# Kernel optimization log

Hardware: AMD Instinct MI355X
Metric: run time of the kernel (lower is better)

## Reference

```python
import jax, jax.numpy as jnp
import numpy as np

B, S, E, H = 2, 2048, 1024, 16
D = E // H  # head_dim = 64


def setup_inputs() -> dict:
    key = jax.random.key(0)
    ks = jax.random.split(key, 9)
    s = 1.0 / np.sqrt(E)
    return {
        "x": jax.random.normal(ks[0], (B, S, E), dtype=jnp.float32),
        "Wq": jax.random.uniform(ks[1], (E, E), jnp.float32, -s, s),
        "bq": jax.random.uniform(ks[2], (E,), jnp.float32, -s, s),
        "Wk": jax.random.uniform(ks[3], (E, E), jnp.float32, -s, s),
        "bk": jax.random.uniform(ks[4], (E,), jnp.float32, -s, s),
        "Wv": jax.random.uniform(ks[5], (E, E), jnp.float32, -s, s),
        "bv": jax.random.uniform(ks[6], (E,), jnp.float32, -s, s),
        "Wo": jax.random.uniform(ks[7], (E, E), jnp.float32, -s, s),
        "bo": jax.random.uniform(ks[8], (E,), jnp.float32, -s, s),
    }


def reference(x, Wq, bq, Wk, bk, Wv, bv, Wo, bo):
    # QKV projections (torch Linear: x @ W.T + b), split into heads: [B,H,S,D]
    def proj(t, W, b):
        return (t @ W.T + b).reshape(B, S, H, D).transpose(0, 2, 1, 3)

    Q = proj(x, Wq, bq)
    K = proj(x, Wk, bk)
    V = proj(x, Wv, bv)
    # scores [B,H,S,S], scaled by sqrt(head_dim)
    score = jnp.einsum('bnqd,bnkd->bnqk', Q, K) / jnp.sqrt(jnp.float32(D))
    weights = jax.nn.softmax(score, axis=-1)
    out = jnp.einsum('bnql,bnld->bnqd', weights, V)  # [B,H,S,D]
    out = out.transpose(0, 2, 1, 3).reshape(B, S, E)
    return out @ Wo.T + bo
```

## Files before the change

kernel.cpp:

```cpp
#include <hip/hip_runtime.h>


#define B_ 2
#define S_ 2048
#define E_ 1024
#define H_ 16
#define D_ 64
#define M_ (B_ * S_)

typedef __attribute__((ext_vector_type(8))) _Float16 f16x8;
typedef __attribute__((ext_vector_type(4))) _Float16 f16x4;
typedef __attribute__((ext_vector_type(2))) _Float16 f16x2;
typedef __attribute__((ext_vector_type(4))) float f32x4;
typedef __attribute__((ext_vector_type(16))) float f32x16;
typedef __attribute__((ext_vector_type(8))) unsigned short u16x8;
typedef __attribute__((ext_vector_type(4))) unsigned int u32x4;

#define LOG2E  1.44269504f
#define CLOG2  4.32808512f

#define KROW 144
#define KBUF 9216
#define VBASE 18432
#define SMEMSZ 36864

static __device__ __forceinline__ float bf16_to_f32(unsigned short u) {
    return __uint_as_float(((unsigned)u) << 16);
}
static __device__ __forceinline__ unsigned short f32_to_bf16(float f) {
    unsigned u = __float_as_uint(f);
    u += 0x7FFFu + ((u >> 16) & 1u);
    return (unsigned short)(u >> 16);
}
static __device__ __forceinline__ float load1_f32(const void* p, int i, bool isbf) {
    return isbf ? bf16_to_f32(((const unsigned short*)p)[i]) : ((const float*)p)[i];
}
static __device__ __forceinline__ void store1(void* p, size_t i, float v, bool isbf) {
    if (isbf) ((unsigned short*)p)[i] = f32_to_bf16(v);
    else      ((float*)p)[i] = v;
}
static __device__ __forceinline__ void gl2lds16(const void* g, void* l) {
    __builtin_amdgcn_global_load_lds((const __attribute__((address_space(1))) unsigned int*)g,
                                     (__attribute__((address_space(3))) unsigned int*)l, 16, 0, 0);
}
static __device__ __forceinline__ float rexp2(float x) {
    float r;
    asm("v_exp_f32 %0, %1" : "=v"(r) : "v"(x));
    return r;
}
static __device__ __forceinline__ unsigned pk2(float a, float b) {
    return __builtin_bit_cast(unsigned, __builtin_amdgcn_cvt_pkrtz(a, b));
}

__global__ __launch_bounds__(256) void convert_inputs(
    const void* __restrict__ x,  const void* __restrict__ wq,
    const void* __restrict__ wk, const void* __restrict__ wv,
    const void* __restrict__ wo,
    _Float16* __restrict__ x16, _Float16* __restrict__ w16,
    int* __restrict__ flag_out)
{
    __shared__ int sflag;
    const int tid = threadIdx.x;
    if (tid < 64) {
        const unsigned short hh = ((const unsigned short*)x)[2 * tid];
        const int e = (hh >> 7) & 0xFF;
        const bool sane = (e >= 0x60 && e <= 0x9F);
        const unsigned long long m = __ballot(sane);
        if (tid == 0) sflag = (__popcll(m) >= 48) ? 1 : 0;
    }
    __syncthreads();
    const bool isbf = sflag != 0;
    if (blockIdx.x == 0 && tid == 0) *flag_out = sflag;

    const size_t t = ((size_t)blockIdx.x * 256 + tid) * 8;
    const void* src; size_t off; _Float16* dst; float scale = 1.0f;
    if (t < (size_t)M_ * E_) { src = x; off = t; dst = x16 + t; }
    else {
        const size_t u = t - (size_t)M_ * E_;
        const int wsel = (int)(u >> 20);
        off = u & ((1u << 20) - 1);
        src = wsel == 0 ? wq : wsel == 1 ? wk : wsel == 2 ? wv : wo;
        dst = w16 + u;
        if (wsel == 0) scale = 0.125f * LOG2E;
    }
    f16x8 v;
    if (isbf) {
        u16x8 s = *(const u16x8*)((const unsigned short*)src + off);
        #pragma unroll
        for (int j = 0; j < 8; ++j) v[j] = (_Float16)(bf16_to_f32(s[j]) * scale);
    } else {
        const float* f = (const float*)src + off;
        f32x4 lo = *(const f32x4*)f;
        f32x4 hi = *(const f32x4*)(f + 4);
        #pragma unroll
        for (int j = 0; j < 4; ++j) {
            v[j]     = (_Float16)(lo[j] * scale);
            v[4 + j] = (_Float16)(hi[j] * scale);
        }
    }
    *(f16x8*)dst = v;
}

__global__ __launch_bounds__(256) void gemm_qkv(
    const _Float16* __restrict__ x16, const _Float16* __restrict__ w16,
    const void* __restrict__ bq, const void* __restrict__ bk, const void* __restrict__ bv,
    const int* __restrict__ flag,
    _Float16* __restrict__ Qb, _Float16* __restrict__ Kb, _Float16* __restrict__ VTb)
{
    __shared__ __align__(16) _Float16 Xs[128 * 64];
    __shared__ __align__(16) _Float16 Ws[64 * 64];
    const bool isbf = (*flag != 0);
    const int tid = threadIdx.x, wave = tid >> 6, lane = tid & 63;
    const int wm = wave >> 1, wn = wave & 1;
    const int qd = lane >> 4, ln = lane & 15;
    const int m0 = blockIdx.x * 128;
    const int by = blockIdx.y;
    const int wsel = by >> 4;
    const int n0 = (by & 15) * 64;
    const _Float16* W = w16 + ((size_t)wsel << 20);

    const _Float16* gx[4]; char* lx[4];
    #pragma unroll
    for (int it = 0; it < 4; ++it) {
        const int seg = it * 256 + tid;
        const int row = seg >> 3, cg = seg & 7;
        const int scol = ((cg + row) & 7) * 8;
        gx[it] = x16 + (size_t)(m0 + row) * E_ + scol;
        lx[it] = (char*)Xs + (size_t)(it * 256 + wave * 64) * 16;
    }
    const _Float16* gw[2]; char* lw[2];
    #pragma unroll
    for (int it = 0; it < 2; ++it) {
        const int seg = it * 256 + tid;
        const int row = seg >> 3, cg = seg & 7;
        const int scol = ((cg + row) & 7) * 8;
        gw[it] = W + (size_t)(n0 + row) * E_ + scol;
        lw[it] = (char*)Ws + (size_t)(it * 256 + wave * 64) * 16;
    }

    const int sw0 = ((qd - ln) & 7) * 8;
    const int sw1 = ((qd + 4 - ln) & 7) * 8;

    f32x4 acc[8] = {};

    for (int kt = 0; kt < E_; kt += 64) {
        __syncthreads();
        #pragma unroll
        for (int it = 0; it < 4; ++it) gl2lds16(gx[it] + kt, lx[it]);
        #pragma unroll
        for (int it = 0; it < 2; ++it) gl2lds16(gw[it] + kt, lw[it]);
        __syncthreads();
        if (wsel != 2) {
            #pragma unroll
            for (int kk = 0; kk < 2; ++kk) {
                const int sw = kk ? sw1 : sw0;
                f16x8 a[4], bfr[2];
                #pragma unroll
                for (int mt = 0; mt < 4; ++mt)
                    a[mt] = *(const f16x8*)&Xs[((wm * 64 + mt * 16 + ln) << 6) + sw];
                #pragma unroll
                for (int nt = 0; nt < 2; ++nt)
                    bfr[nt] = *(const f16x8*)&Ws[((wn * 32 + nt * 16 + ln) << 6) + sw];
                #pragma unroll
                for (int mt = 0; mt < 4; ++mt)
                    #pragma unroll
                    for (int nt = 0; nt < 2; ++nt)
                        acc[mt * 2 + nt] = __builtin_amdgcn_mfma_f32_16x16x32_f16(a[mt], bfr[nt], acc[mt * 2 + nt], 0, 0, 0);
            }
        } else {
            #pragma unroll
            for (int kk = 0; kk < 2; ++kk) {
                const int sw = kk ? sw1 : sw0;
                f16x8 a[2], bfr[4];
                #pragma unroll
                for (int mt = 0; mt < 2; ++mt)
                    a[mt] = *(const f16x8*)&Ws[((wm * 32 + mt * 16 + ln) << 6) + sw];
                #pragma unroll
                for (int nt = 0; nt < 4; ++nt)
                    bfr[nt] = *(const f16x8*)&Xs[((wn * 64 + nt * 16 + ln) << 6) + sw];
                #pragma unroll
                for (int mt = 0; mt < 2; ++mt)
                    #pragma unroll
                    for (int nt = 0; nt < 4; ++nt)
                        acc[mt * 4 + nt] = __builtin_amdgcn_mfma_f32_16x16x32_f16(a[mt], bfr[nt], acc[mt * 4 + nt], 0, 0, 0);
            }
        }
    }

    if (wsel != 2) {
        const void* bias = wsel == 0 ? bq : bk;
        const float bscale = (wsel == 0) ? 0.125f * LOG2E : 1.0f;
        _Float16* dst = wsel == 0 ? Qb : Kb;
        #pragma unroll
        for (int nt = 0; nt < 2; ++nt) {
            const int n = n0 + wn * 32 + nt * 16 + ln;
            const float bvv = load1_f32(bias, n, isbf) * bscale;
            const int h = n >> 6, d = n & 63;
            #pragma unroll
            for (int mt = 0; mt < 4; ++mt)
                #pragma unroll
                for (int r = 0; r < 4; ++r) {
                    const int m = m0 + wm * 64 + mt * 16 + qd * 4 + r;
                    const int b = m >> 11, s = m & (S_ - 1);
                    dst[((size_t)(b * H_ + h) * S_ + s) * D_ + d] =
                        (_Float16)(acc[mt * 2 + nt][r] + bvv);
                }
        }
    } else {
        #pragma unroll
        for (int mt = 0; mt < 2; ++mt)
            #pragma unroll
            for (int r = 0; r < 4; ++r) {
                const int e = n0 + wm * 32 + mt * 16 + qd * 4 + r;
                const float bvv = load1_f32(bv, e, isbf);
                const int h = e >> 6, d = e & 63;
                #pragma unroll
                for (int nt = 0; nt < 4; ++nt) {
                    const int sg = m0 + wn * 64 + nt * 16 + ln;
                    const int b = sg >> 11, s = sg & (S_ - 1);
                    VTb[((size_t)(b * H_ + h) * D_ + d) * S_ + s] =
                        (_Float16)(acc[mt * 4 + nt][r] + bvv);
                }
            }
    }
}

__global__ __launch_bounds__(256, 4) void attn(
    const _Float16* __restrict__ Q, const _Float16* __restrict__ K,
    const _Float16* __restrict__ VT, _Float16* __restrict__ AO)
{
    __shared__ __align__(16) char smem[SMEMSZ];

    const int tid = threadIdx.x, wave = tid >> 6, lane = tid & 63;
    const int rl = lane & 31, h = lane >> 5;
    const int qg = wave & 1, kh = wave >> 1;
    const int L = blockIdx.x;
    const int bh = ((L & 7) << 2) | ((L >> 3) & 3);
    const int qt = L >> 5;
    const int b = bh >> 4, hh = bh & (H_ - 1);

    const _Float16* Kbase = K + (size_t)bh * S_ * D_;
    const _Float16* Vbase = VT + (size_t)bh * D_ * S_;

    f16x8 qf[4];
    {
        const _Float16* qrow = Q + ((size_t)bh * S_ + qt * 64 + qg * 32 + rl) * D_ + h * 8;
        #pragma unroll
        for (int c = 0; c < 4; ++c) qf[c] = *(const f16x8*)(qrow + c * 16);
    }

    const _Float16* kg[2]; const _Float16* vg[2]; int swk[2], swv[2];
    #pragma unroll
    for (int it = 0; it < 2; ++it) {
        const int seg = it * 256 + tid;
        const int row = seg >> 3, c = seg & 7;
        kg[it] = Kbase + (size_t)row * D_ + c * 8;
        vg[it] = Vbase + (size_t)row * S_ + c * 8;
        swk[it] = row * KROW + c * 16;
        swv[it] = row * KROW + (c >> 1) * 32 + (c & 1) * 8;
    }

    int koff[4];
    #pragma unroll
    for (int c = 0; c < 4; ++c)
        koff[c] = (kh * 32 + rl) * KROW + (((c << 1) | h) << 4);
    const int vrow0 = rl * KROW, vrow1 = (32 + rl) * KROW;
    const int vcol = h * 16;

    f32x16 o0 = {}, o1 = {};
    float lisum = 0.0f;

    {
        f16x8 kr[2], vr[2];
        #pragma unroll
        for (int it = 0; it < 2; ++it) { kr[it] = *(const f16x8*)kg[it]; vr[it] = *(const f16x8*)vg[it]; }
        #pragma unroll
        for (int it = 0; it < 2; ++it) {
            *(f16x8*)(smem + swk[it]) = kr[it];
            *(f16x4*)(smem + VBASE + swv[it])      = __builtin_shufflevector(vr[it], vr[it], 0, 1, 2, 3);
            *(f16x4*)(smem + VBASE + swv[it] + 16) = __builtin_shufflevector(vr[it], vr[it], 4, 5, 6, 7);
        }
    }
    __syncthreads();

    for (int kt = 0; kt < S_; kt += 64) {
        const int p = (kt >> 6) & 1;
        const bool more = (kt + 64) < S_;

        f16x8 kr[2], vr[2];
        if (more) {
            #pragma unroll
            for (int it = 0; it < 2; ++it) {
                kr[it] = *(const f16x8*)(kg[it] + (size_t)(kt + 64) * D_);
                vr[it] = *(const f16x8*)(vg[it] + (kt + 64));
            }
        }

        const char* kb = smem + p * KBUF;
        const char* vb = smem + VBASE + p * KBUF;

        f16x8 af[4];
        #pragma unroll
        for (int c = 0; c < 4; ++c) af[c] = *(const f16x8*)(kb + koff[c]);

        f32x16 sc = {};
        __builtin_amdgcn_s_setprio(1);
        #pragma unroll
        for (int c = 0; c < 4; ++c)
            sc = __builtin_amdgcn_mfma_f32_32x32x16_f16(af[c], qf[c], sc, 0, 0, 0);
        __builtin_amdgcn_s_setprio(0);

        float e[16];
        #pragma unroll
        for (int i = 0; i < 16; ++i) e[i] = rexp2(sc[i] - CLOG2);

        lisum += (((e[0] + e[1]) + (e[2] + e[3])) + ((e[4] + e[5]) + (e[6] + e[7])))
               + (((e[8] + e[9]) + (e[10] + e[11])) + ((e[12] + e[13]) + (e[14] + e[15])));

        #pragma unroll
        for (int ks = 0; ks < 2; ++ks) {
            const int oo = 8 * ks;
            const f16x8 pf = __builtin_bit_cast(f16x8, (u32x4){
                pk2(e[oo + 0], e[oo + 1]), pk2(e[oo + 2], e[oo + 3]),
                pk2(e[oo + 4], e[oo + 5]), pk2(e[oo + 6], e[oo + 7])});

            const int go = ((kh * 2 + ks) << 5) + vcol;
            const f16x8 v0 = *(const f16x8*)(vb + vrow0 + go);
            const f16x8 v1 = *(const f16x8*)(vb + vrow1 + go);

            __builtin_amdgcn_s_setprio(1);
            o0 = __builtin_amdgcn_mfma_f32_32x32x16_f16(pf, v0, o0, 0, 0, 0);
            o1 = __builtin_amdgcn_mfma_f32_32x32x16_f16(pf, v1, o1, 0, 0, 0);
            __builtin_amdgcn_s_setprio(0);
        }

        if (more) {
            #pragma unroll
            for (int it = 0; it < 2; ++it) {
                *(f16x8*)(smem + (p ^ 1) * KBUF + swk[it]) = kr[it];
                *(f16x4*)(smem + VBASE + (p ^ 1) * KBUF + swv[it])      = __builtin_shufflevector(vr[it], vr[it], 0, 1, 2, 3);
                *(f16x4*)(smem + VBASE + (p ^ 1) * KBUF + swv[it] + 16) = __builtin_shufflevector(vr[it], vr[it], 4, 5, 6, 7);
            }
        }
        __syncthreads();
    }

    float* red = (float*)smem;
    float* lig = (float*)(smem + 16384);
    const int rbase = qg * 64 + lane;
    lig[(qg * 32 + rl) * 4 + kh * 2 + h] = lisum;
    if (kh) {
        #pragma unroll
        for (int i = 0; i < 16; ++i) {
            red[i * 128 + rbase]        = o0[i];
            red[(16 + i) * 128 + rbase] = o1[i];
        }
    }
    __syncthreads();
    if (!kh) {
        #pragma unroll
        for (int i = 0; i < 16; ++i) {
            const float t0 = o0[i] + red[i * 128 + rbase];
            const float t1 = o1[i] + red[(16 + i) * 128 + rbase];
            const int ql = qg * 32 + 4 * h + (i & 3) + 8 * (i >> 2);
            const f32x4 lv = *(const f32x4*)&lig[ql * 4];
            const float inv = 1.0f / ((lv[0] + lv[1]) + (lv[2] + lv[3]));
            const int q = qt * 64 + ql;
            _Float16* dst = AO + ((size_t)b * S_ + q) * E_ + hh * D_;
            dst[rl]      = (_Float16)(t0 * inv);
            dst[32 + rl] = (_Float16)(t1 * inv);
        }
    }
}

__global__ __launch_bounds__(256) void gemm_out(
    const _Float16* __restrict__ A, const _Float16* __restrict__ W,
    const void* __restrict__ bias, const int* __restrict__ flag, void* __restrict__ out)
{
    __shared__ __align__(16) _Float16 As[128 * 64];
    __shared__ __align__(16) _Float16 Bs[64 * 64];
    const bool isbf = (*flag != 0);
    const int tid = threadIdx.x, wave = tid >> 6, lane = tid & 63;
    const int wm = wave >> 1, wn = wave & 1;
    const int qd = lane >> 4, ln = lane & 15;
    const int m0 = blockIdx.x * 128;
    const int n0 = blockIdx.y * 64;

    const _Float16* ga[4]; char* la[4];
    #pragma unroll
    for (int it = 0; it < 4; ++it) {
        const int seg = it * 256 + tid;
        const int row = seg >> 3, cg = seg & 7;
        const int scol = ((cg + row) & 7) * 8;
        ga[it] = A + (size_t)(m0 + row) * E_ + scol;
        la[it] = (char*)As + (size_t)(it * 256 + wave * 64) * 16;
    }
    const _Float16* gb[2]; char* lb[2];
    #pragma unroll
    for (int it = 0; it < 2; ++it) {
        const int seg = it * 256 + tid;
        const int row = seg >> 3, cg = seg & 7;
        const int scol = ((cg + row) & 7) * 8;
        gb[it] = W + (size_t)(n0 + row) * E_ + scol;
        lb[it] = (char*)Bs + (size_t)(it * 256 + wave * 64) * 16;
    }
    const int sw0 = ((qd - ln) & 7) * 8;
    const int sw1 = ((qd + 4 - ln) & 7) * 8;

    f32x4 acc[8] = {};

    for (int kt = 0; kt < E_; kt += 64) {
        __syncthreads();
        #pragma unroll
        for (int it = 0; it < 4; ++it) gl2lds16(ga[it] + kt, la[it]);
        #pragma unroll
        for (int it = 0; it < 2; ++it) gl2lds16(gb[it] + kt, lb[it]);
        __syncthreads();
        #pragma unroll
        for (int kk = 0; kk < 2; ++kk) {
            const int sw = kk ? sw1 : sw0;
            f16x8 a[4], bfr[2];
            #pragma unroll
            for (int mt = 0; mt < 4; ++mt)
                a[mt] = *(const f16x8*)&As[((wm * 64 + mt * 16 + ln) << 6) + sw];
            #pragma unroll
            for (int nt = 0; nt < 2; ++nt)
                bfr[nt] = *(const f16x8*)&Bs[((wn * 32 + nt * 16 + ln) << 6) + sw];
            #pragma unroll
            for (int mt = 0; mt < 4; ++mt)
                #pragma unroll
                for (int nt = 0; nt < 2; ++nt)
                    acc[mt * 2 + nt] = __builtin_amdgcn_mfma_f32_16x16x32_f16(a[mt], bfr[nt], acc[mt * 2 + nt], 0, 0, 0);
        }
    }

    #pragma unroll
    for (int nt = 0; nt < 2; ++nt) {
        const int n = n0 + wn * 32 + nt * 16 + ln;
        const float bvv = load1_f32(bias, n, isbf);
        #pragma unroll
        for (int mt = 0; mt < 4; ++mt)
            #pragma unroll
            for (int r = 0; r < 4; ++r) {
                const int m = m0 + wm * 64 + mt * 16 + qd * 4 + r;
                store1(out, (size_t)m * E_ + n, acc[mt * 2 + nt][r] + bvv, isbf);
            }
    }
}

extern "C" void kernel_launch(void* const* d_in, const int* in_sizes, int n_in,
                              void* d_out, int out_size, void* d_ws, size_t ws_size,
                              hipStream_t stream) {
    const void* x  = d_in[0];
    const void* Wq = d_in[1];
    const void* bq = d_in[2];
    const void* Wk = d_in[3];
    const void* bk = d_in[4];
    const void* Wv = d_in[5];
    const void* bv = d_in[6];
    const void* Wo = d_in[7];
    const void* bo = d_in[8];

    int* flag = (int*)d_ws;
    _Float16* x16 = (_Float16*)((char*)d_ws + 1024);
    _Float16* w16 = x16 + (size_t)M_ * E_;
    _Float16* Qb  = w16 + 4u * (size_t)E_ * E_;
    _Float16* Kb  = Qb + (size_t)M_ * E_;
    _Float16* VTb = Kb + (size_t)M_ * E_;
    _Float16* AO  = x16;

    convert_inputs<<<4096, 256, 0, stream>>>(x, Wq, Wk, Wv, Wo, x16, w16, flag);
    gemm_qkv<<<dim3(32, 48), 256, 0, stream>>>(x16, w16, bq, bk, bv, flag, Qb, Kb, VTb);
    attn<<<1024, 256, 0, stream>>>(Qb, Kb, VTb, AO);
    gemm_out<<<dim3(32, 16), 256, 0, stream>>>(AO, w16 + 3u * (size_t)E_ * E_, bo, flag, d_out);
}
```

Before: 194.0 us.

## Load V directly from global into registers in attention; shrink out-proj GEMM tile

The attention kernel no longer stages V^T tiles through shared memory. Each lane loads its f16x4 V fragments straight from global memory, which halves LDS use (SMEMSZ drops to 18432) and removes the V LDS stores and reads. The cost is uncoalesced, non-prefetched global loads inside the inner loop. Separately, the output projection GEMM tile is reduced from 128x64 to 64x64, doubling the grid to 1024 blocks for better CU occupancy, at the price of more redundant weight loads.

```diff
diff --git a/kernel.cpp b/kernel.cpp
--- a/kernel.cpp
+++ b/kernel.cpp
@@ -21,8 +21,7 @@
 
 #define KROW 144
 #define KBUF 9216
-#define VBASE 18432
-#define SMEMSZ 36864
+#define SMEMSZ 18432
 
 static __device__ __forceinline__ float bf16_to_f32(unsigned short u) {
     return __uint_as_float(((unsigned)u) << 16);
@@ -249,37 +248,32 @@
         for (int c = 0; c < 4; ++c) qf[c] = *(const f16x8*)(qrow + c * 16);
     }
 
-    const _Float16* kg[2]; const _Float16* vg[2]; int swk[2], swv[2];
+    const _Float16* kg[2]; int swk[2];
     #pragma unroll
     for (int it = 0; it < 2; ++it) {
         const int seg = it * 256 + tid;
         const int row = seg >> 3, c = seg & 7;
         kg[it] = Kbase + (size_t)row * D_ + c * 8;
-        vg[it] = Vbase + (size_t)row * S_ + c * 8;
         swk[it] = row * KROW + c * 16;
-        swv[it] = row * KROW + (c >> 1) * 32 + (c & 1) * 8;
     }
 
     int koff[4];
     #pragma unroll
     for (int c = 0; c < 4; ++c)
         koff[c] = (kh * 32 + rl) * KROW + (((c << 1) | h) << 4);
-    const int vrow0 = rl * KROW, vrow1 = (32 + rl) * KROW;
-    const int vcol = h * 16;
+
+    const _Float16* vp0 = Vbase + (size_t)rl * S_ + kh * 32 + h * 4;
+    const _Float16* vp1 = Vbase + (size_t)(32 + rl) * S_ + kh * 32 + h * 4;
 
     f32x16 o0 = {}, o1 = {};
     float lisum = 0.0f;
 
     {
-        f16x8 kr[2], vr[2];
-        #pragma unroll
-        for (int it = 0; it < 2; ++it) { kr[it] = *(const f16x8*)kg[it]; vr[it] = *(const f16x8*)vg[it]; }
-        #pragma unroll
-        for (int it = 0; it < 2; ++it) {
-            *(f16x8*)(smem + swk[it]) = kr[it];
-            *(f16x4*)(smem + VBASE + swv[it])      = __builtin_shufflevector(vr[it], vr[it], 0, 1, 2, 3);
-            *(f16x4*)(smem + VBASE + swv[it] + 16) = __builtin_shufflevector(vr[it], vr[it], 4, 5, 6, 7);
-        }
+        f16x8 kr[2];
+        #pragma unroll
+        for (int it = 0; it < 2; ++it) kr[it] = *(const f16x8*)kg[it];
+        #pragma unroll
+        for (int it = 0; it < 2; ++it) *(f16x8*)(smem + swk[it]) = kr[it];
     }
     __syncthreads();
 
@@ -287,18 +281,24 @@
         const int p = (kt >> 6) & 1;
         const bool more = (kt + 64) < S_;
 
-        f16x8 kr[2], vr[2];
+        f16x8 kr[2];
         if (more) {
             #pragma unroll
-            for (int it = 0; it < 2; ++it) {
+            for (int it = 0; it < 2; ++it)
                 kr[it] = *(const f16x8*)(kg[it] + (size_t)(kt + 64) * D_);
-                vr[it] = *(const f16x8*)(vg[it] + (kt + 64));
-            }
+        }
+        f16x4 va[8];
+        #pragma unroll
+        for (int ks = 0; ks < 2; ++ks) {
+            const _Float16* c0 = vp0 + kt + ks * 16;
+            const _Float16* c1 = vp1 + kt + ks * 16;
+            va[ks * 4 + 0] = *(const f16x4*)c0;
+            va[ks * 4 + 1] = *(const f16x4*)(c0 + 8);
+            va[ks * 4 + 2] = *(const f16x4*)c1;
+            va[ks * 4 + 3] = *(const f16x4*)(c1 + 8);
         }
 
         const char* kb = smem + p * KBUF;
-        const char* vb = smem + VBASE + p * KBUF;
-
         f16x8 af[4];
         #pragma unroll
         for (int c = 0; c < 4; ++c) af[c] = *(const f16x8*)(kb + koff[c]);
@@ -324,9 +324,8 @@
                 pk2(e[oo + 0], e[oo + 1]), pk2(e[oo + 2], e[oo + 3]),
                 pk2(e[oo + 4], e[oo + 5]), pk2(e[oo + 6], e[oo + 7])});
 
-            const int go = ((kh * 2 + ks) << 5) + vcol;
-            const f16x8 v0 = *(const f16x8*)(vb + vrow0 + go);
-            const f16x8 v1 = *(const f16x8*)(vb + vrow1 + go);
+            const f16x8 v0 = __builtin_shufflevector(va[ks * 4 + 0], va[ks * 4 + 1], 0, 1, 2, 3, 4, 5, 6, 7);
+            const f16x8 v1 = __builtin_shufflevector(va[ks * 4 + 2], va[ks * 4 + 3], 0, 1, 2, 3, 4, 5, 6, 7);
 
             __builtin_amdgcn_s_setprio(1);
             o0 = __builtin_amdgcn_mfma_f32_32x32x16_f16(pf, v0, o0, 0, 0, 0);
@@ -336,11 +335,8 @@
 
         if (more) {
             #pragma unroll
-            for (int it = 0; it < 2; ++it) {
+            for (int it = 0; it < 2; ++it)
                 *(f16x8*)(smem + (p ^ 1) * KBUF + swk[it]) = kr[it];
-                *(f16x4*)(smem + VBASE + (p ^ 1) * KBUF + swv[it])      = __builtin_shufflevector(vr[it], vr[it], 0, 1, 2, 3);
-                *(f16x4*)(smem + VBASE + (p ^ 1) * KBUF + swv[it] + 16) = __builtin_shufflevector(vr[it], vr[it], 4, 5, 6, 7);
-            }
         }
         __syncthreads();
     }
@@ -377,57 +373,52 @@
     const _Float16* __restrict__ A, const _Float16* __restrict__ W,
     const void* __restrict__ bias, const int* __restrict__ flag, void* __restrict__ out)
 {
-    __shared__ __align__(16) _Float16 As[128 * 64];
+    __shared__ __align__(16) _Float16 As[64 * 64];
     __shared__ __align__(16) _Float16 Bs[64 * 64];
     const bool isbf = (*flag != 0);
     const int tid = threadIdx.x, wave = tid >> 6, lane = tid & 63;
     const int wm = wave >> 1, wn = wave & 1;
     const int qd = lane >> 4, ln = lane & 15;
-    const int m0 = blockIdx.x * 128;
+    const int m0 = blockIdx.x * 64;
     const int n0 = blockIdx.y * 64;
 
-    const _Float16* ga[4]; char* la[4];
-    #pragma unroll
-    for (int it = 0; it < 4; ++it) {
+    const _Float16* ga[2]; char* la[2];
+    const _Float16* gb[2]; char* lb[2];
+    #pragma unroll
+    for (int it = 0; it < 2; ++it) {
         const int seg = it * 256 + tid;
         const int row = seg >> 3, cg = seg & 7;
         const int scol = ((cg + row) & 7) * 8;
         ga[it] = A + (size_t)(m0 + row) * E_ + scol;
+        gb[it] = W + (size_t)(n0 + row) * E_ + scol;
         la[it] = (char*)As + (size_t)(it * 256 + wave * 64) * 16;
-    }
-    const _Float16* gb[2]; char* lb[2];
-    #pragma unroll
-    for (int it = 0; it < 2; ++it) {
-        const int seg = it * 256 + tid;
-        const int row = seg >> 3, cg = seg & 7;
-        const int scol = ((cg + row) & 7) * 8;
-        gb[it] = W + (size_t)(n0 + row) * E_ + scol;
         lb[it] = (char*)Bs + (size_t)(it * 256 + wave * 64) * 16;
     }
     const int sw0 = ((qd - ln) & 7) * 8;
     const int sw1 = ((qd + 4 - ln) & 7) * 8;
 
-    f32x4 acc[8] = {};
+    f32x4 acc[4] = {};
 
     for (int kt = 0; kt < E_; kt += 64) {
         __syncthreads();
         #pragma unroll
-        for (int it = 0; it < 4; ++it) gl2lds16(ga[it] + kt, la[it]);
-        #pragma unroll
-        for (int it = 0; it < 2; ++it) gl2lds16(gb[it] + kt, lb[it]);
+        for (int it = 0; it < 2; ++it) {
+            gl2lds16(ga[it] + kt, la[it]);
+            gl2lds16(gb[it] + kt, lb[it]);
+        }
         __syncthreads();
         #pragma unroll
         for (int kk = 0; kk < 2; ++kk) {
             const int sw = kk ? sw1 : sw0;
-            f16x8 a[4], bfr[2];
-            #pragma unroll
-            for (int mt = 0; mt < 4; ++mt)
-                a[mt] = *(const f16x8*)&As[((wm * 64 + mt * 16 + ln) << 6) + sw];
+            f16x8 a[2], bfr[2];
+            #pragma unroll
+            for (int mt = 0; mt < 2; ++mt)
+                a[mt] = *(const f16x8*)&As[((wm * 32 + mt * 16 + ln) << 6) + sw];
             #pragma unroll
             for (int nt = 0; nt < 2; ++nt)
                 bfr[nt] = *(const f16x8*)&Bs[((wn * 32 + nt * 16 + ln) << 6) + sw];
             #pragma unroll
-            for (int mt = 0; mt < 4; ++mt)
+            for (int mt = 0; mt < 2; ++mt)
                 #pragma unroll
                 for (int nt = 0; nt < 2; ++nt)
                     acc[mt * 2 + nt] = __builtin_amdgcn_mfma_f32_16x16x32_f16(a[mt], bfr[nt], acc[mt * 2 + nt], 0, 0, 0);
@@ -439,10 +430,10 @@
         const int n = n0 + wn * 32 + nt * 16 + ln;
         const float bvv = load1_f32(bias, n, isbf);
         #pragma unroll
-        for (int mt = 0; mt < 4; ++mt)
+        for (int mt = 0; mt < 2; ++mt)
             #pragma unroll
             for (int r = 0; r < 4; ++r) {
-                const int m = m0 + wm * 64 + mt * 16 + qd * 4 + r;
+                const int m = m0 + wm * 32 + mt * 16 + qd * 4 + r;
                 store1(out, (size_t)m * E_ + n, acc[mt * 2 + nt][r] + bvv, isbf);
             }
     }
@@ -472,5 +463,5 @@
     convert_inputs<<<4096, 256, 0, stream>>>(x, Wq, Wk, Wv, Wo, x16, w16, flag);
     gemm_qkv<<<dim3(32, 48), 256, 0, stream>>>(x16, w16, bq, bk, bv, flag, Qb, Kb, VTb);
     attn<<<1024, 256, 0, stream>>>(Qb, Kb, VTb, AO);
-    gemm_out<<<dim3(32, 16), 256, 0, stream>>>(AO, w16 + 3u * (size_t)E_ * E_, bo, flag, d_out);
-}
+    gemm_out<<<dim3(64, 16), 256, 0, stream>>>(AO, w16 + 3u * (size_t)E_ * E_, bo, flag, d_out);
+}
```

After: 267.0 us. +37.6%, slower.
